# Performance work log

Measured on AMD Instinct MI355X. Metric: run time of the kernel, lower is better.

## Reference

```python
import jax, jax.numpy as jnp
import numpy as np

H = W = 28
B = 16384


def _make_masks():
    # pixel groups: 4 interleaved checkerboard-like groups over the 28x28 grid
    pg = np.zeros([4, H, W], np.float32)
    pg[0, ::2, ::2] = 1
    pg[1, 1::2, 1::2] = 1
    pg[2, ::2, 1::2] = 1
    pg[3, 1::2, ::2] = 1
    pcg = pg[:, None]  # [4,1,28,28] (dims[0]=1 channel)
    # information mask x = sum of pixel_channel_groups[:x] (cumulative, exclusive)
    info = np.stack([pcg[:x].sum(0) if x > 0 else np.zeros([1, H, W], np.float32)
                     for x in range(4)])  # [4,1,28,28]
    return jnp.asarray(info), jnp.asarray(pcg)


def setup_inputs() -> dict:
    key = jax.random.key(0)
    k1, k2, k3, k4 = jax.random.split(key, 4)
    samples = jax.random.bernoulli(k1, 0.5, (B, 1, H, W)).astype(jnp.float32)
    position = 0.01 * jax.random.normal(k2, (1, H, W), dtype=jnp.float32)
    weights = 0.1 * jax.random.normal(k3, (4, 1, 2, 3, 3), dtype=jnp.float32)
    biases = 0.1 * jax.random.normal(k4, (4, 1), dtype=jnp.float32)
    return {"samples": samples, "position": position,
            "weights": weights, "biases": biases}


def reference(samples, position, weights, biases):
    info, pcg = _make_masks()
    # position layer broadcast to [B,1,H,W]
    pos = jnp.broadcast_to(position[None], samples.shape)

    def branch(w, b, im, pm):
        # masked input || position channel -> [B,2,H,W]
        inp = jnp.concatenate([samples * im, pos], axis=1)
        logits = jax.lax.conv_general_dilated(
            inp, w, window_strides=(1, 1), padding='SAME',
            dimension_numbers=('NCHW', 'OIHW', 'NCHW')) + b[None, :, None, None]
        # Bernoulli(logits).log_prob(x) = x*logits - softplus(logits)
        lp = samples * logits - jax.nn.softplus(logits)
        return jnp.sum(pm * lp)

    totals = jax.vmap(branch)(weights, biases, info, pcg)  # [4]
    return jnp.sum(totals)
```

## Files before the change

kernel.cpp:

```cpp
#include <hip/hip_runtime.h>


#define GRID 2048

__device__ __forceinline__ float sp_fast(float x) {
    return __logf(1.0f + __expf(x));
}

__device__ __forceinline__ float pos_logit(const float* __restrict__ pos,
                                           const float* __restrict__ w,
                                           const float* __restrict__ b,
                                           int x, int h, int ww) {
    float s = b[x];
    #pragma unroll
    for (int ky = 0; ky < 3; ++ky) {
        #pragma unroll
        for (int kx = 0; kx < 3; ++kx) {
            int hh = h + ky - 1, cc = ww + kx - 1;
            float p = (hh >= 0 && hh < 28 && cc >= 0 && cc < 28) ? pos[hh*28 + cc] : 0.0f;
            s = fmaf(w[x*18 + 9 + ky*3 + kx], p, s);
        }
    }
    return s;
}

__global__ void prep_kernel(const float* __restrict__ pos,
                            const float* __restrict__ w,
                            const float* __restrict__ b,
                            float* __restrict__ tbl) {
    int u = blockIdx.x * blockDim.x + threadIdx.x;
    int t = u >> 2, x = u & 3;
    int i = t / 14, j = t % 14;
    bool valid = (t < 196);
    if (x == 0) {
        float C0 = 0.f, S0 = 0.f;
        if (valid) { C0 = pos_logit(pos, w, b, 0, 2*i, 2*j); S0 = sp_fast(C0); }
        tbl[t*8 + 0] = C0; tbl[t*8 + 1] = S0;
    } else if (x == 1) {
        tbl[t*8 + 2] = valid ? pos_logit(pos, w, b, 1, 2*i+1, 2*j+1) : 0.f;
        tbl[t*8 + 5] = 0.f;
    } else if (x == 2) {
        tbl[t*8 + 3] = valid ? pos_logit(pos, w, b, 2, 2*i,   2*j+1) : 0.f;
        tbl[t*8 + 6] = 0.f;
    } else {
        tbl[t*8 + 4] = valid ? pos_logit(pos, w, b, 3, 2*i+1, 2*j) : 0.f;
        tbl[t*8 + 7] = 0.f;
    }
}

__global__ __launch_bounds__(256, 4)
void main_kernel(const float* __restrict__ samples,
                 const float* __restrict__ w,
                 const float* __restrict__ tbl,
                 float* __restrict__ partial) {
    __shared__ float2 planes[4][1024];
    const int tid = threadIdx.x;
    const int wv = tid >> 6, ln = tid & 63;
    float2* myP = planes[wv];

    const float w1a = w[18+0], w1b = w[18+2], w1c = w[18+6], w1d = w[18+8];
    const float w2l = w[36+3], w2r = w[36+5], w2u = w[36+1], w2n = w[36+7];
    const float w3u = w[54+1], w3n = w[54+7], w3l = w[54+3], w3r = w[54+5];
    const float w3a = w[54+0], w3b = w[54+2], w3c = w[54+6], w3e = w[54+8];

    float C0[4], P1[4], P2[4], P3[4], S0s = 0.f;
    int oq[4], wo[4]; bool qv[4];
    #pragma unroll
    for (int k = 0; k < 4; ++k) {
        int t = k*64 + ln;
        qv[k] = (t < 196);
        int i = t / 14, j = t - 14*i;
        oq[k] = (i+1)*16 + (j+1);
        const float4* t4 = (const float4*)(tbl + t*8);
        float4 lo = t4[0], hi = t4[1];
        C0[k] = lo.x; S0s += lo.y; P1[k] = lo.z; P2[k] = lo.w; P3[k] = hi.x;
        int r = t / 7, m = t - 7*r;
        wo[k] = ((r & 1) ? 512 : 0) + ((r >> 1) + 1)*16 + 2*m + 1;
    }

    #pragma unroll
    for (int z = 0; z < 8; ++z)
        ((float4*)myP)[z*64 + ln] = float4{0.f, 0.f, 0.f, 0.f};

    float acc = -2.0f * S0s;
    const int img0 = blockIdx.x * 8 + wv * 2;
    const float4* src0 = (const float4*)(samples + (size_t)img0 * 784);
    const float4* src1 = (const float4*)(samples + (size_t)(img0 + 1) * 784);

    float4 v0[4], v1[4];
    #pragma unroll
    for (int k = 0; k < 4; ++k)
        if (k < 3 || ln < 4) {
            v0[k] = src0[k*64 + ln];
            v1[k] = src1[k*64 + ln];
        }
    __builtin_amdgcn_wave_barrier();
    #pragma unroll
    for (int k = 0; k < 4; ++k)
        if (k < 3 || ln < 4) {
            float2* p = myP + wo[k];
            p[0]   = float2{v0[k].x, v1[k].x};
            p[1]   = float2{v0[k].z, v1[k].z};
            p[256] = float2{v0[k].y, v1[k].y};
            p[257] = float2{v0[k].w, v1[k].w};
        }
    __builtin_amdgcn_wave_barrier();

    auto quad_ll = [&](float a00, float a01, float a10, float a11,
                       float bl,  float bij, float bdl, float bdn,
                       float cij, float dup, float dl,  float dij,
                       float c0,  float p1,  float p2,  float p3) {
        acc = fmaf(a00, c0, acc);
        float L1 = p1;
        L1 = fmaf(w1a, a00, L1); L1 = fmaf(w1b, a01, L1);
        L1 = fmaf(w1c, a10, L1); L1 = fmaf(w1d, a11, L1);
        acc += fmaf(dij, L1, -sp_fast(L1));
        float L2 = p2;
        L2 = fmaf(w2l, a00, L2); L2 = fmaf(w2r, a01, L2);
        L2 = fmaf(w2u, dup, L2); L2 = fmaf(w2n, dij, L2);
        acc += fmaf(bij, L2, -sp_fast(L2));
        float L3 = p3;
        L3 = fmaf(w3u, a00, L3); L3 = fmaf(w3n, a10, L3);
        L3 = fmaf(w3l, dl,  L3); L3 = fmaf(w3r, dij, L3);
        L3 = fmaf(w3a, bl,  L3); L3 = fmaf(w3b, bij, L3);
        L3 = fmaf(w3c, bdl, L3); L3 = fmaf(w3e, bdn, L3);
        acc += fmaf(cij, L3, -sp_fast(L3));
    };

    #pragma unroll
    for (int k = 0; k < 4; ++k) {
        if (qv[k]) {
            const int o = oq[k];
            float2 A00 = myP[o],        A01 = myP[o+1];
            float2 A10 = myP[o+16],     A11 = myP[o+17];
            float2 Bl  = myP[256+o-1],  Bij = myP[256+o];
            float2 Bdl = myP[256+o+15], Bdn = myP[256+o+16];
            float2 Cij = myP[512+o];
            float2 Dup = myP[768+o-16], Dl  = myP[768+o-1], Dij = myP[768+o];
            quad_ll(A00.x,A01.x,A10.x,A11.x, Bl.x,Bij.x,Bdl.x,Bdn.x,
                    Cij.x,Dup.x,Dl.x,Dij.x, C0[k],P1[k],P2[k],P3[k]);
            quad_ll(A00.y,A01.y,A10.y,A11.y, Bl.y,Bij.y,Bdl.y,Bdn.y,
                    Cij.y,Dup.y,Dl.y,Dij.y, C0[k],P1[k],P2[k],P3[k]);
        }
    }

    #pragma unroll
    for (int off = 32; off >= 1; off >>= 1)
        acc += __shfl_xor(acc, off, 64);
    if (ln == 0) partial[blockIdx.x * 4 + wv] = acc;
}

__global__ void final_kernel(const float* __restrict__ partial,
                             float* __restrict__ out) {
    __shared__ float red[4];
    const int tid = threadIdx.x;
    float s = 0.f;
    #pragma unroll
    for (int i = 0; i < 32; ++i) s += partial[i*256 + tid];
    #pragma unroll
    for (int off = 32; off >= 1; off >>= 1) s += __shfl_xor(s, off, 64);
    if ((tid & 63) == 0) red[tid >> 6] = s;
    __syncthreads();
    if (tid == 0) out[0] = red[0] + red[1] + red[2] + red[3];
}

extern "C" void kernel_launch(void* const* d_in, const int* in_sizes, int n_in,
                              void* d_out, int out_size, void* d_ws, size_t ws_size,
                              hipStream_t stream) {
    const float* samples  = (const float*)d_in[0];
    const float* position = (const float*)d_in[1];
    const float* weights  = (const float*)d_in[2];
    const float* biases   = (const float*)d_in[3];
    float* ws_f = (float*)d_ws;
    float* tbl     = ws_f;
    float* partial = ws_f + 2048;
    float* out = (float*)d_out;

    prep_kernel<<<4, 256, 0, stream>>>(position, weights, biases, tbl);
    main_kernel<<<GRID, 256, 0, stream>>>(samples, weights, tbl, partial);
    final_kernel<<<1, 256, 0, stream>>>(partial, out);
}
```

Measured before the change: 97.46 us.

## Fuse position-logit table prep into main kernel and reduce per block

Removes the separate prep kernel launch by having every block recompute the position-dependent logit table into shared memory before staging samples. Each block also reduces its four wave sums in shared memory and writes one partial instead of four, so the final kernel reads fewer values. This saves a launch and a dependency between kernels, but adds redundant 3x3 conv work and extra __syncthreads in each of the 2048 blocks.

```diff
diff --git a/kernel.cpp b/kernel.cpp
--- a/kernel.cpp
+++ b/kernel.cpp
@@ -24,39 +24,35 @@
     return s;
 }
 
-__global__ void prep_kernel(const float* __restrict__ pos,
-                            const float* __restrict__ w,
-                            const float* __restrict__ b,
-                            float* __restrict__ tbl) {
-    int u = blockIdx.x * blockDim.x + threadIdx.x;
-    int t = u >> 2, x = u & 3;
-    int i = t / 14, j = t % 14;
-    bool valid = (t < 196);
-    if (x == 0) {
-        float C0 = 0.f, S0 = 0.f;
-        if (valid) { C0 = pos_logit(pos, w, b, 0, 2*i, 2*j); S0 = sp_fast(C0); }
-        tbl[t*8 + 0] = C0; tbl[t*8 + 1] = S0;
-    } else if (x == 1) {
-        tbl[t*8 + 2] = valid ? pos_logit(pos, w, b, 1, 2*i+1, 2*j+1) : 0.f;
-        tbl[t*8 + 5] = 0.f;
-    } else if (x == 2) {
-        tbl[t*8 + 3] = valid ? pos_logit(pos, w, b, 2, 2*i,   2*j+1) : 0.f;
-        tbl[t*8 + 6] = 0.f;
-    } else {
-        tbl[t*8 + 4] = valid ? pos_logit(pos, w, b, 3, 2*i+1, 2*j) : 0.f;
-        tbl[t*8 + 7] = 0.f;
-    }
-}
-
 __global__ __launch_bounds__(256, 4)
 void main_kernel(const float* __restrict__ samples,
                  const float* __restrict__ w,
-                 const float* __restrict__ tbl,
+                 const float* __restrict__ pos,
+                 const float* __restrict__ b,
                  float* __restrict__ partial) {
     __shared__ float2 planes[4][1024];
+    __shared__ float red[4];
+    float* tbl = (float*)planes;
     const int tid = threadIdx.x;
     const int wv = tid >> 6, ln = tid & 63;
     float2* myP = planes[wv];
+
+    #pragma unroll
+    for (int r = 0; r < 4; ++r) {
+        int idx = r*256 + tid;
+        if (idx < 980) {
+            int s = idx / 196, t = idx - 196*s;
+            int i = t / 14, j = t - 14*i;
+            float val;
+            if      (s == 0) val = pos_logit(pos, w, b, 0, 2*i,   2*j);
+            else if (s == 1) val = sp_fast(pos_logit(pos, w, b, 0, 2*i, 2*j));
+            else if (s == 2) val = pos_logit(pos, w, b, 1, 2*i+1, 2*j+1);
+            else if (s == 3) val = pos_logit(pos, w, b, 2, 2*i,   2*j+1);
+            else             val = pos_logit(pos, w, b, 3, 2*i+1, 2*j);
+            tbl[idx] = val;
+        }
+    }
+    __syncthreads();
 
     const float w1a = w[18+0], w1b = w[18+2], w1c = w[18+6], w1d = w[18+8];
     const float w2l = w[36+3], w2r = w[36+5], w2u = w[36+1], w2n = w[36+7];
@@ -71,12 +67,14 @@
         qv[k] = (t < 196);
         int i = t / 14, j = t - 14*i;
         oq[k] = (i+1)*16 + (j+1);
-        const float4* t4 = (const float4*)(tbl + t*8);
-        float4 lo = t4[0], hi = t4[1];
-        C0[k] = lo.x; S0s += lo.y; P1[k] = lo.z; P2[k] = lo.w; P3[k] = hi.x;
+        if (qv[k]) {
+            C0[k] = tbl[t];        S0s  += tbl[196+t];
+            P1[k] = tbl[392+t];    P2[k] = tbl[588+t];   P3[k] = tbl[784+t];
+        } else { C0[k] = P1[k] = P2[k] = P3[k] = 0.f; }
         int r = t / 7, m = t - 7*r;
         wo[k] = ((r & 1) ? 512 : 0) + ((r >> 1) + 1)*16 + 2*m + 1;
     }
+    __syncthreads();
 
     #pragma unroll
     for (int z = 0; z < 8; ++z)
@@ -147,7 +145,9 @@
     #pragma unroll
     for (int off = 32; off >= 1; off >>= 1)
         acc += __shfl_xor(acc, off, 64);
-    if (ln == 0) partial[blockIdx.x * 4 + wv] = acc;
+    if (ln == 0) red[wv] = acc;
+    __syncthreads();
+    if (tid == 0) partial[blockIdx.x] = red[0] + red[1] + red[2] + red[3];
 }
 
 __global__ void final_kernel(const float* __restrict__ partial,
@@ -156,7 +156,7 @@
     const int tid = threadIdx.x;
     float s = 0.f;
     #pragma unroll
-    for (int i = 0; i < 32; ++i) s += partial[i*256 + tid];
+    for (int i = 0; i < 8; ++i) s += partial[i*256 + tid];
     #pragma unroll
     for (int off = 32; off >= 1; off >>= 1) s += __shfl_xor(s, off, 64);
     if ((tid & 63) == 0) red[tid >> 6] = s;
@@ -171,12 +171,9 @@
     const float* position = (const float*)d_in[1];
     const float* weights  = (const float*)d_in[2];
     const float* biases   = (const float*)d_in[3];
-    float* ws_f = (float*)d_ws;
-    float* tbl     = ws_f;
-    float* partial = ws_f + 2048;
+    float* partial = (float*)d_ws;
     float* out = (float*)d_out;
 
-    prep_kernel<<<4, 256, 0, stream>>>(position, weights, biases, tbl);
-    main_kernel<<<GRID, 256, 0, stream>>>(samples, weights, tbl, partial);
+    main_kernel<<<GRID, 256, 0, stream>>>(samples, weights, position, biases, partial);
     final_kernel<<<1, 256, 0, stream>>>(partial, out);
 }
```

Measured after the change: 100.6 us. 3.2% more time.
